# Kernel tuning notes

Measured on AMD Instinct MI355X. Metric: run time of the kernel, lower is better.

The kernel has to match this reference:

```python
import jax, jax.numpy as jnp
import numpy as np

DEPTH = 3

def _rx(theta):
    c, s = jnp.cos(theta / 2), jnp.sin(theta / 2)
    return jnp.stack([jnp.stack([c + 0j, -1j * s], -1),
                      jnp.stack([-1j * s, c + 0j], -1)], -2)

def _ry(theta):
    c, s = jnp.cos(theta / 2), jnp.sin(theta / 2)
    return jnp.stack([jnp.stack([c + 0j, -s + 0j], -1),
                      jnp.stack([s + 0j, c + 0j], -1)], -2)

def _rz(theta):
    e = jnp.exp(-0.5j * theta.astype(jnp.complex64))
    z = jnp.zeros_like(e)
    return jnp.stack([jnp.stack([e, z], -1),
                      jnp.stack([z, jnp.conj(e)], -1)], -2)

def _apply_1q(state, U, q):
    # state: (batch, 2,2,...,2); wire q lives on axis q+1. U: (2,2) or (batch,2,2)
    s = jnp.moveaxis(state, q + 1, -1)
    if U.ndim == 3:
        s = jnp.einsum('b...i,bji->b...j', s, U)
    else:
        s = jnp.einsum('...i,ji->...j', s, U)
    return jnp.moveaxis(s, -1, q + 1)

def _apply_cnot(state, c, t):
    s = jnp.moveaxis(state, (c + 1, t + 1), (-2, -1))
    s = jnp.concatenate([s[..., 0:1, :], s[..., 1:2, ::-1]], axis=-2)
    return jnp.moveaxis(s, (-2, -1), (c + 1, t + 1))

def _circuit(x, params):
    batch, n = x.shape
    depth = params.shape[0]
    state = jnp.zeros((batch,) + (2,) * n, jnp.complex64)
    state = state.at[(slice(None),) + (0,) * n].set(1.0)
    # data-encoding RX with per-sample angles
    for q in range(n):
        state = _apply_1q(state, _rx(x[:, q].astype(jnp.complex64).real), q)
    for l in range(depth):
        for q in range(n):
            state = _apply_1q(state, _rx(params[l, q, 0]), q)
            state = _apply_1q(state, _ry(params[l, q, 1]), q)
            state = _apply_1q(state, _rz(params[l, q, 2]), q)
        for q in range(n - 1):
            state = _apply_cnot(state, q, q + 1)
        state = _apply_cnot(state, n - 1, 0)
    probs = state.real ** 2 + state.imag ** 2  # (batch, 2,...,2)
    exps = []
    for w in range(n):
        p = jnp.moveaxis(probs, w + 1, 1).reshape(batch, 2, -1).sum(-1)
        exps.append(p[:, 0] - p[:, 1])  # <Z_w> = P(0) - P(1)
    return jnp.stack(exps, axis=1)


def setup_inputs() -> dict:
    key = jax.random.key(0)
    k1, k2 = jax.random.split(key)
    batch, n = 128, 14
    x = jax.random.normal(k1, (batch, n), dtype=jnp.float32)
    params = jax.random.normal(k2, (DEPTH, n, 3), dtype=jnp.float32)
    return {"x": x, "params": params}


def reference(x, params):
    return _circuit(x, params)
```

## Files before the change

kernel.cpp:

```cpp
#include <hip/hip_runtime.h>

namespace {

using v2f = __attribute__((ext_vector_type(2))) float;

constexpr int NQ      = 14;
constexpr int NSTATES = 1 << NQ;
constexpr int BLOCK   = 1024;
constexpr int NWAVES  = BLOCK / 64;

constexpr unsigned cparity(unsigned x){ x^=x>>8; x^=x>>4; x^=x>>2; x^=x>>1; return x&1u; }

struct Mat { unsigned row[NQ]; unsigned col[NQ]; };

constexpr Mat m_after(int nr){
  Mat m{};
  for(int p=0;p<NQ;++p){ m.row[p]=1u<<p; m.col[p]=1u<<p; }
  for(int l=0;l<nr;++l)
    for(int q=0;q<NQ;++q){
      int cq=(q==NQ-1)?NQ-1:q, tq=(q==NQ-1)?0:q+1;
      int Pc=NQ-1-cq, Pt=NQ-1-tq;
      m.row[Pt]^=m.row[Pc]; m.col[Pc]^=m.col[Pt];
    }
  return m;
}

constexpr Mat M1=m_after(1), M2=m_after(2), M3=m_after(3);
constexpr unsigned amask(int q){ return M1.col[NQ-1-q]; }
constexpr unsigned arow (int q){ return M1.row[NQ-1-q]; }
constexpr unsigned bmask(int q){ return M2.col[NQ-1-q]; }
constexpr unsigned brow (int q){ return M2.row[NQ-1-q]; }

constexpr int rank_of(const unsigned* v, int n){
  unsigned a[24]{};
  for(int i=0;i<n;++i) a[i]=v[i];
  int r=0;
  for(int bit=15;bit>=0;--bit){
    int p=-1;
    for(int i=r;i<n;++i){ if((a[i]>>bit)&1){ p=i; break; } }
    if(p<0) continue;
    unsigned t=a[r]; a[r]=a[p]; a[p]=t;
    for(int i=0;i<n;++i) if(i!=r && ((a[i]>>bit)&1)) a[i]^=a[r];
    ++r;
  }
  return r;
}

constexpr unsigned swzf(unsigned s, int k){ return s ^ ((s>>k)&31u); }

constexpr int proj_rank4(const unsigned* cols, int n, int k){
  unsigned a[8]{};
  for(int i=0;i<n;++i) a[i]=swzf(cols[i],k)&15u;
  int r=0;
  for(int bit=3;bit>=0;--bit){
    int p=-1;
    for(int i=r;i<n;++i){ if((a[i]>>bit)&1){ p=i; break; } }
    if(p<0) continue;
    unsigned t=a[r]; a[r]=a[p]; a[p]=t;
    for(int i=0;i<n;++i) if(i!=r && ((a[i]>>bit)&1)) a[i]^=a[r];
    ++r;
  }
  return r;
}

struct Plan {
  unsigned A[14], B[14], C[14];
  int BlaneGi[6]; unsigned BlanePi4[6];
  int BregGi[4];  unsigned BregEps[4];
  int CregGi[4];  unsigned CregEps[4];
  int ClaneGi[4]; unsigned ClaneEps[4];
  unsigned EJ4[14], ET[14];
  int K;
  unsigned SA[16], SB[16], SC[16];
  unsigned TA[10], TB[10], TCc[10];
};

constexpr Plan make_plan(){
  Plan P{};
  for(int t=0;t<14;++t) P.A[t]=amask(t);
  for(int t=0;t<4;++t){ P.B[t]=amask(10+t); P.BregGi[t]=10+t; }
  bool used[14]{}; int picked[14]{}; int np=0;
  {
    unsigned cur[20]{}; int nc=0;
    for(int t=0;t<4;++t) cur[nc++]=P.B[t];
    for(int q=0;q<14 && np<10;++q){
      cur[nc]=bmask(q);
      if(rank_of(cur,nc+1)==nc+1){ ++nc; picked[np++]=q; used[q]=true; }
    }
  }
  for(int i=0;i<6;++i){ P.B[4+i]=bmask(picked[i]); P.BlaneGi[i]=14+picked[i]; }
  int wq[4]{}, un[4]{}; int nu=0;
  for(int i=0;i<4;++i){ wq[i]=picked[6+i]; P.B[10+i]=bmask(wq[i]); P.CregGi[i]=14+wq[i]; }
  for(int q=0;q<14;++q) if(!used[q]) un[nu++]=q;
  for(int i=0;i<4;++i) P.ClaneGi[i]=14+un[i];
  for(int i=0;i<4;++i){ unsigned m=0;
    for(int t=0;t<10;++t) m |= cparity(arow(10+i)&P.B[4+t])<<t;
    P.BregEps[i]=m; }
  for(int i=0;i<6;++i){ unsigned m=0;
    for(int t=0;t<4;++t) m |= cparity(brow(picked[i])&P.B[t])<<t;
    P.BlanePi4[i]=m; }
  for(int t=0;t<4;++t) P.C[t]=bmask(wq[t]);
  for(int t=0;t<4;++t) P.C[4+t]=bmask(un[t]);
  {
    unsigned cc[20]{}; int n=0;
    for(int t=0;t<8;++t) cc[n++]=P.C[t];
    int pos=8;
    for(int p=0;p<14 && pos<14;++p){
      cc[n]=1u<<p;
      if(rank_of(cc,n+1)==n+1){ P.C[pos]=1u<<p; ++n; ++pos; }
    }
  }
  for(int i=0;i<4;++i){ unsigned m=0;
    for(int t=0;t<10;++t) m |= cparity(brow(wq[i])&P.C[4+t])<<t;
    P.CregEps[i]=m; }
  for(int i=0;i<4;++i){ unsigned m=0;
    for(int t=0;t<10;++t){ if(t==i) continue; m |= cparity(brow(un[i])&P.C[4+t])<<t; }
    P.ClaneEps[i]=m; }
  for(int w=0;w<14;++w){
    unsigned R=M3.row[NQ-1-w]; unsigned mj=0, mt=0;
    for(int t=0;t<4;++t)  mj |= cparity(R&P.C[t])<<t;
    for(int t=0;t<10;++t) mt |= cparity(R&P.C[4+t])<<t;
    P.EJ4[w]=mj; P.ET[w]=mt;
  }
  int bestk=2, bests=-1;
  for(int k=2;k<=9;++k){
    unsigned ini[6]={16,32,64,128,256,512};
    int s = proj_rank4(ini,6,k) + proj_rank4(&P.A[4],6,k)
          + proj_rank4(&P.B[4],6,k) + proj_rank4(&P.C[4],6,k);
    if(s>bests){ bests=s; bestk=k; }
  }
  P.K=bestk;
  for(int j=0;j<16;++j){
    unsigned sa=0, sb=0, sc=0;
    for(int t=0;t<4;++t) if((j>>t)&1){ sa^=P.A[t]; sb^=P.B[t]; sc^=P.C[t]; }
    P.SA[j]=swzf(sa,bestk); P.SB[j]=swzf(sb,bestk); P.SC[j]=swzf(sc,bestk);
  }
  for(int t=0;t<10;++t){
    P.TA[t]=swzf(P.A[4+t],bestk);
    P.TB[t]=swzf(P.B[4+t],bestk);
    P.TCc[t]=swzf(P.C[4+t],bestk);
  }
  return P;
}

constexpr Plan PL = make_plan();
static_assert(rank_of(PL.A,14)==14, "phase A map not bijective");
static_assert(rank_of(PL.B,14)==14, "phase B map not bijective");
static_assert(rank_of(PL.C,14)==14, "phase C map not bijective");

__device__ __forceinline__ v2f mkv(float a, float b){ v2f r; r[0]=a; r[1]=b; return r; }

__device__ __forceinline__ v2f pk_mul(v2f a, v2f b){
  v2f d; asm("v_pk_mul_f32 %0, %1, %2 op_sel:[0,0] op_sel_hi:[1,1]" : "=v"(d) : "v"(a), "v"(b)); return d;
}
__device__ __forceinline__ v2f pk_fma(v2f a, v2f b, v2f c){
  v2f d; asm("v_pk_fma_f32 %0, %1, %2, %3 op_sel:[0,0,0] op_sel_hi:[1,1,1]" : "=v"(d) : "v"(a), "v"(b), "v"(c)); return d;
}
__device__ __forceinline__ v2f pk_fma_swap1(v2f a, v2f b, v2f c){
  v2f d; asm("v_pk_fma_f32 %0, %1, %2, %3 op_sel:[0,1,0] op_sel_hi:[1,0,1]" : "=v"(d) : "v"(a), "v"(b), "v"(c)); return d;
}
__device__ __forceinline__ v2f cmul_pk(v2f uxx, v2f uyn, v2f s){ return pk_fma_swap1(uyn, s, pk_mul(uxx, s)); }
__device__ __forceinline__ v2f cfma_pk(v2f uxx, v2f uyn, v2f s, v2f acc){ return pk_fma_swap1(uyn, s, pk_fma(uxx, s, acc)); }

__device__ __forceinline__ float2 cmulf(float2 a, float2 b){
  return make_float2(a.x*b.x - a.y*b.y, a.x*b.y + a.y*b.x);
}
__device__ __forceinline__ v2f sel2(bool c, v2f x, v2f y){ v2f r; r[0]=c?x[0]:y[0]; r[1]=c?x[1]:y[1]; return r; }

struct GC { v2f u00x,u00n,u01x,u01n,u10x,u10n,u11x,u11n; };
__device__ __forceinline__ GC load_gc(const v2f* __restrict__ g){
  GC c{g[0],g[1],g[2],g[3],g[4],g[5],g[6],g[7]}; return c;
}

template<int KIND, int CTRL>
__device__ __forceinline__ v2f xchg(v2f v, int bpa){
  int x0=__float_as_int(v[0]), x1=__float_as_int(v[1]);
  int y0, y1;
  if constexpr (KIND==0){
    y0=__builtin_amdgcn_update_dpp(0,x0,CTRL,0xF,0xF,true);
    y1=__builtin_amdgcn_update_dpp(0,x1,CTRL,0xF,0xF,true);
  } else if constexpr (KIND==1){
    y0=__builtin_amdgcn_ds_swizzle(x0,CTRL);
    y1=__builtin_amdgcn_ds_swizzle(x1,CTRL);
  } else {
    y0=__builtin_amdgcn_ds_bpermute(bpa,x0);
    y1=__builtin_amdgcn_ds_bpermute(bpa,x1);
  }
  v2f r; r[0]=__int_as_float(y0); r[1]=__int_as_float(y1); return r;
}

template<int BIT>
__device__ __forceinline__ void reg_gate(v2f (&a)[16], const GC& c, bool eps){
  v2f m00x=sel2(eps,c.u11x,c.u00x), m00n=sel2(eps,c.u11n,c.u00n);
  v2f m01x=sel2(eps,c.u10x,c.u01x), m01n=sel2(eps,c.u10n,c.u01n);
  v2f m10x=sel2(eps,c.u01x,c.u10x), m10n=sel2(eps,c.u01n,c.u10n);
  v2f m11x=sel2(eps,c.u00x,c.u11x), m11n=sel2(eps,c.u00n,c.u11n);
#pragma unroll
  for(int v=0; v<16; ++v){
    if(!((v>>BIT)&1)){
      int w = v | (1<<BIT);
      v2f a0=a[v], a1=a[w];
      a[v] = cfma_pk(m01x,m01n,a1, cmul_pk(m00x,m00n,a0));
      a[w] = cfma_pk(m11x,m11n,a1, cmul_pk(m10x,m10n,a0));
    }
  }
}

template<int KIND, int CTRL, unsigned PI4>
__device__ __forceinline__ void lane_gate(v2f (&a)[16], const GC& c, bool sel, int bpa){
  v2f kax0=sel2(sel,c.u11x,c.u00x), kan0=sel2(sel,c.u11n,c.u00n);
  v2f kbx0=sel2(sel,c.u10x,c.u01x), kbn0=sel2(sel,c.u10n,c.u01n);
  v2f kax1=sel2(sel,c.u00x,c.u11x), kan1=sel2(sel,c.u00n,c.u11n);
  v2f kbx1=sel2(sel,c.u01x,c.u10x), kbn1=sel2(sel,c.u01n,c.u10n);
#pragma unroll
  for(int j=0;j<16;++j){
    v2f th = xchg<KIND,CTRL>(a[j], bpa);
    bool pi = (__builtin_popcount(PI4 & (unsigned)j) & 1) != 0;
    v2f kax = pi?kax1:kax0, kan = pi?kan1:kan0;
    v2f kbx = pi?kbx1:kbx0, kbn = pi?kbn1:kbn0;
    a[j] = cfma_pk(kbx,kbn,th, cmul_pk(kax,kan,a[j]));
  }
}

__device__ __forceinline__ unsigned base10(unsigned tid, const unsigned (&tc)[10]){
  unsigned s=0;
#pragma unroll
  for(int t=0;t<10;++t) s ^= tc[t] & (0u - ((tid>>t)&1u));
  return s;
}

__global__ void prep_gates(const float* __restrict__ prm, float* __restrict__ wsf){
  int t = threadIdx.x;
  if(t >= 2*NQ) return;
  int l = 1 + t/NQ, q = t % NQ;
  float ax=prm[(l*NQ+q)*3+0], ay=prm[(l*NQ+q)*3+1], az=prm[(l*NQ+q)*3+2];
  float cx,sx,cy,sy,cz,sz;
  sincosf(0.5f*ax,&sx,&cx); sincosf(0.5f*ay,&sy,&cy); sincosf(0.5f*az,&sz,&cz);
  float2 M00=make_float2(cy*cx, sy*sx),  M01=make_float2(-sy*cx,-cy*sx);
  float2 M10=make_float2(sy*cx,-cy*sx),  M11=make_float2(cy*cx,-sy*sx);
  float2 ez =make_float2(cz,-sz), ezc=make_float2(cz,sz);
  float2 U00=cmulf(ez,M00), U01=cmulf(ez,M01), U10=cmulf(ezc,M10), U11=cmulf(ezc,M11);
  float* o = wsf + t*16;
  o[0]=U00.x; o[1]=U00.x; o[2]=-U00.y; o[3]=U00.y;
  o[4]=U01.x; o[5]=U01.x; o[6]=-U01.y; o[7]=U01.y;
  o[8]=U10.x; o[9]=U10.x; o[10]=-U10.y; o[11]=U10.y;
  o[12]=U11.x; o[13]=U11.x; o[14]=-U11.y; o[15]=U11.y;
}

__global__ __launch_bounds__(BLOCK, 4) void qsim_kernel(
    const float* __restrict__ x,
    const float* __restrict__ prm,
    const v2f*  __restrict__ gw,
    float* __restrict__ out)
{
  __shared__ v2f    st[NSTATES];
  __shared__ float2 l0c[NQ][2];
  __shared__ float  red[NWAVES][NQ];

  const int b   = blockIdx.x;
  const unsigned tid = threadIdx.x;
  const int bpa = (int)((((tid&63u)^32u)<<2));

  if(tid < NQ){
    int q = tid;
    float ax = prm[q*3+0] + x[b*NQ+q];
    float ay = prm[q*3+1], az = prm[q*3+2];
    float cx,sx,cy,sy,cz,sz;
    sincosf(0.5f*ax,&sx,&cx); sincosf(0.5f*ay,&sy,&cy); sincosf(0.5f*az,&sz,&cz);
    l0c[q][0] = cmulf(make_float2(cz,-sz), make_float2(cy*cx,  sy*sx));
    l0c[q][1] = cmulf(make_float2(cz, sz), make_float2(sy*cx, -cy*sx));
  }
  __syncthreads();

  {
    float2 Pk = l0c[0][(tid>>9)&1];
#pragma unroll
    for(int q=1;q<10;++q) Pk = cmulf(Pk, l0c[q][(tid>>(9-q))&1]);
    float2 t2[2], t4[4];
    t2[0]=cmulf(Pk,l0c[10][0]); t2[1]=cmulf(Pk,l0c[10][1]);
#pragma unroll
    for(int i=0;i<2;++i){ t4[2*i]=cmulf(t2[i],l0c[11][0]); t4[2*i+1]=cmulf(t2[i],l0c[11][1]); }
#pragma unroll
    for(int j=0;j<16;++j){
      float2 v = cmulf(cmulf(t4[j>>2], l0c[12][(j>>1)&1]), l0c[13][j&1]);
      unsigned s = (tid<<4) | (unsigned)j;
      unsigned slot = s ^ ((s>>PL.K)&31u);
      st[slot] = mkv(v.x, v.y);
    }
  }
  __syncthreads();

  {
    unsigned sb = base10(tid, PL.TA);
    v2f a[16];
#pragma unroll
    for(int j=0;j<16;++j) a[j] = st[sb ^ PL.SA[j]];
    reg_gate<0>(a, load_gc(gw+0*8), false);
    reg_gate<1>(a, load_gc(gw+1*8), false);
    reg_gate<2>(a, load_gc(gw+2*8), false);
    reg_gate<3>(a, load_gc(gw+3*8), false);
    lane_gate<0,0xB1,  0u>(a, load_gc(gw+4*8), (tid&1)!=0,  bpa);
    lane_gate<0,0x4E,  0u>(a, load_gc(gw+5*8), (tid&2)!=0,  bpa);
    lane_gate<1,0x101F,0u>(a, load_gc(gw+6*8), (tid&4)!=0,  bpa);
    lane_gate<1,0x201F,0u>(a, load_gc(gw+7*8), (tid&8)!=0,  bpa);
    lane_gate<1,0x401F,0u>(a, load_gc(gw+8*8), (tid&16)!=0, bpa);
    lane_gate<2,0,     0u>(a, load_gc(gw+9*8), (tid&32)!=0, bpa);
#pragma unroll
    for(int j=0;j<16;++j) st[sb ^ PL.SA[j]] = a[j];
  }
  __syncthreads();

  {
    unsigned sb = base10(tid, PL.TB);
    v2f a[16];
#pragma unroll
    for(int j=0;j<16;++j) a[j] = st[sb ^ PL.SB[j]];
    reg_gate<0>(a, load_gc(gw+PL.BregGi[0]*8), (__builtin_popcount(PL.BregEps[0]&tid)&1)!=0);
    reg_gate<1>(a, load_gc(gw+PL.BregGi[1]*8), (__builtin_popcount(PL.BregEps[1]&tid)&1)!=0);
    reg_gate<2>(a, load_gc(gw+PL.BregGi[2]*8), (__builtin_popcount(PL.BregEps[2]&tid)&1)!=0);
    reg_gate<3>(a, load_gc(gw+PL.BregGi[3]*8), (__builtin_popcount(PL.BregEps[3]&tid)&1)!=0);
    lane_gate<0,0xB1,  PL.BlanePi4[0]>(a, load_gc(gw+PL.BlaneGi[0]*8), (tid&1)!=0,  bpa);
    lane_gate<0,0x4E,  PL.BlanePi4[1]>(a, load_gc(gw+PL.BlaneGi[1]*8), (tid&2)!=0,  bpa);
    lane_gate<1,0x101F,PL.BlanePi4[2]>(a, load_gc(gw+PL.BlaneGi[2]*8), (tid&4)!=0,  bpa);
    lane_gate<1,0x201F,PL.BlanePi4[3]>(a, load_gc(gw+PL.BlaneGi[3]*8), (tid&8)!=0,  bpa);
    lane_gate<1,0x401F,PL.BlanePi4[4]>(a, load_gc(gw+PL.BlaneGi[4]*8), (tid&16)!=0, bpa);
    lane_gate<2,0,     PL.BlanePi4[5]>(a, load_gc(gw+PL.BlaneGi[5]*8), (tid&32)!=0, bpa);
#pragma unroll
    for(int j=0;j<16;++j) st[sb ^ PL.SB[j]] = a[j];
  }
  __syncthreads();

  {
    unsigned sb = base10(tid, PL.TCc);
    v2f a[16];
#pragma unroll
    for(int j=0;j<16;++j) a[j] = st[sb ^ PL.SC[j]];
    reg_gate<0>(a, load_gc(gw+PL.CregGi[0]*8), (__builtin_popcount(PL.CregEps[0]&tid)&1)!=0);
    reg_gate<1>(a, load_gc(gw+PL.CregGi[1]*8), (__builtin_popcount(PL.CregEps[1]&tid)&1)!=0);
    reg_gate<2>(a, load_gc(gw+PL.CregGi[2]*8), (__builtin_popcount(PL.CregEps[2]&tid)&1)!=0);
    reg_gate<3>(a, load_gc(gw+PL.CregGi[3]*8), (__builtin_popcount(PL.CregEps[3]&tid)&1)!=0);
    lane_gate<0,0xB1,  0u>(a, load_gc(gw+PL.ClaneGi[0]*8),
        (((tid&1u)!=0) != ((__builtin_popcount(PL.ClaneEps[0]&tid)&1)!=0)), bpa);
    lane_gate<0,0x4E,  0u>(a, load_gc(gw+PL.ClaneGi[1]*8),
        (((tid&2u)!=0) != ((__builtin_popcount(PL.ClaneEps[1]&tid)&1)!=0)), bpa);
    lane_gate<1,0x101F,0u>(a, load_gc(gw+PL.ClaneGi[2]*8),
        (((tid&4u)!=0) != ((__builtin_popcount(PL.ClaneEps[2]&tid)&1)!=0)), bpa);
    lane_gate<1,0x201F,0u>(a, load_gc(gw+PL.ClaneGi[3]*8),
        (((tid&8u)!=0) != ((__builtin_popcount(PL.ClaneEps[3]&tid)&1)!=0)), bpa);

    float acc[NQ];
#pragma unroll
    for(int w=0;w<NQ;++w) acc[w]=0.f;
#pragma unroll
    for(int j=0;j<16;++j){
      float p = a[j][0]*a[j][0] + a[j][1]*a[j][1];
#pragma unroll
      for(int w=0;w<NQ;++w){
        if(__builtin_popcount(PL.EJ4[w] & (unsigned)j) & 1) acc[w]-=p; else acc[w]+=p;
      }
    }
    const int lane = tid & 63, wave = tid >> 6;
#pragma unroll
    for(int w=0;w<NQ;++w){
      float v = (__builtin_popcount(PL.ET[w]&tid)&1) ? -acc[w] : acc[w];
#pragma unroll
      for(int off=32; off>0; off>>=1) v += __shfl_down(v, off, 64);
      if(lane==0) red[wave][w]=v;
    }
    __syncthreads();
    if(tid < NQ){
      float s=0.f;
#pragma unroll
      for(int wv=0; wv<NWAVES; ++wv) s += red[wv][tid];
      out[b*NQ + tid] = s;
    }
  }
}

}

extern "C" void kernel_launch(void* const* d_in, const int* in_sizes, int n_in,
                              void* d_out, int out_size, void* d_ws, size_t ws_size,
                              hipStream_t stream) {
  const float* x   = (const float*)d_in[0];
  const float* prm = (const float*)d_in[1];
  float* out = (float*)d_out;
  const int batch = in_sizes[0] / NQ;
  prep_gates<<<1, 64, 0, stream>>>(prm, (float*)d_ws);
  qsim_kernel<<<batch, BLOCK, 0, stream>>>(x, prm, (const v2f*)d_ws, out);
}
```

Baseline: 42.59 us.

## Replace XOR-swizzled shared state with padded scatter layout and cache gate tables in LDS

Removes the XOR-swizzle addressing of the shared state vector. Each phase now reads its 16 amplitudes contiguously from a row padded to stride 17, then scatters results into the next phase's layout through compile-time inverse basis maps. This needs an extra barrier before each scatter. Gate matrices are staged into shared memory instead of being read from global memory. Lane exchanges switch from ds_bpermute and one ds_swizzle to DPP row_shr-style moves and permlane32_swap, cutting LDS-based shuffles at the cost of a larger shared footprint (17K v2f).

```diff
diff --git a/kernel.cpp b/kernel.cpp
--- a/kernel.cpp
+++ b/kernel.cpp
@@ -46,23 +46,6 @@
   return r;
 }
 
-constexpr unsigned swzf(unsigned s, int k){ return s ^ ((s>>k)&31u); }
-
-constexpr int proj_rank4(const unsigned* cols, int n, int k){
-  unsigned a[8]{};
-  for(int i=0;i<n;++i) a[i]=swzf(cols[i],k)&15u;
-  int r=0;
-  for(int bit=3;bit>=0;--bit){
-    int p=-1;
-    for(int i=r;i<n;++i){ if((a[i]>>bit)&1){ p=i; break; } }
-    if(p<0) continue;
-    unsigned t=a[r]; a[r]=a[p]; a[p]=t;
-    for(int i=0;i<n;++i) if(i!=r && ((a[i]>>bit)&1)) a[i]^=a[r];
-    ++r;
-  }
-  return r;
-}
-
 struct Plan {
   unsigned A[14], B[14], C[14];
   int BlaneGi[6]; unsigned BlanePi4[6];
@@ -70,9 +53,6 @@
   int CregGi[4];  unsigned CregEps[4];
   int ClaneGi[4]; unsigned ClaneEps[4];
   unsigned EJ4[14], ET[14];
-  int K;
-  unsigned SA[16], SB[16], SC[16];
-  unsigned TA[10], TB[10], TCc[10];
 };
 
 constexpr Plan make_plan(){
@@ -122,24 +102,6 @@
     for(int t=0;t<10;++t) mt |= cparity(R&P.C[4+t])<<t;
     P.EJ4[w]=mj; P.ET[w]=mt;
   }
-  int bestk=2, bests=-1;
-  for(int k=2;k<=9;++k){
-    unsigned ini[6]={16,32,64,128,256,512};
-    int s = proj_rank4(ini,6,k) + proj_rank4(&P.A[4],6,k)
-          + proj_rank4(&P.B[4],6,k) + proj_rank4(&P.C[4],6,k);
-    if(s>bests){ bests=s; bestk=k; }
-  }
-  P.K=bestk;
-  for(int j=0;j<16;++j){
-    unsigned sa=0, sb=0, sc=0;
-    for(int t=0;t<4;++t) if((j>>t)&1){ sa^=P.A[t]; sb^=P.B[t]; sc^=P.C[t]; }
-    P.SA[j]=swzf(sa,bestk); P.SB[j]=swzf(sb,bestk); P.SC[j]=swzf(sc,bestk);
-  }
-  for(int t=0;t<10;++t){
-    P.TA[t]=swzf(P.A[4+t],bestk);
-    P.TB[t]=swzf(P.B[4+t],bestk);
-    P.TCc[t]=swzf(P.C[4+t],bestk);
-  }
   return P;
 }
 
@@ -148,6 +110,64 @@
 static_assert(rank_of(PL.B,14)==14, "phase B map not bijective");
 static_assert(rank_of(PL.C,14)==14, "phase C map not bijective");
 
+struct Inv { unsigned col[NQ]; };
+constexpr Inv inv_basis(const unsigned* bas){
+  unsigned vec[NQ]{}, cmb[NQ]{}; bool used[NQ]{}; int pivk[NQ]{};
+  for(int k=0;k<NQ;++k){ vec[k]=bas[k]; cmb[k]=1u<<k; }
+  for(int b=0;b<NQ;++b){
+    int p=-1;
+    for(int k=0;k<NQ;++k) if(!used[k] && ((vec[k]>>b)&1)){ p=k; break; }
+    used[p]=true; pivk[b]=p;
+    for(int k=0;k<NQ;++k) if(k!=p && ((vec[k]>>b)&1)){ vec[k]^=vec[p]; cmb[k]^=cmb[p]; }
+  }
+  Inv R{};
+  for(int b=0;b<NQ;++b) R.col[b]=cmb[pivk[b]];
+  return R;
+}
+constexpr bool check_inv(const unsigned* bas, const Inv& iv){
+  for(int p=0;p<NQ;++p){
+    unsigned s=0;
+    for(int k=0;k<NQ;++k) if((iv.col[p]>>k)&1) s^=bas[k];
+    if(s != (1u<<p)) return false;
+  }
+  return true;
+}
+constexpr Inv IA = inv_basis(PL.A), IB = inv_basis(PL.B), IC = inv_basis(PL.C);
+static_assert(check_inv(PL.A, IA), "IA");
+static_assert(check_inv(PL.B, IB), "IB");
+static_assert(check_inv(PL.C, IC), "IC");
+
+struct Trans { unsigned t[NQ]; };
+constexpr Trans trans_phys(const Inv& iv){
+  Trans T{};
+  for(int p=0;p<NQ;++p) T.t[p]=iv.col[p];
+  return T;
+}
+constexpr Trans trans_of(const unsigned* cur, const Inv& iv){
+  Trans T{};
+  for(int k=0;k<NQ;++k){
+    unsigned c=0;
+    for(int p=0;p<NQ;++p) if((cur[k]>>p)&1) c^=iv.col[p];
+    T.t[k]=c;
+  }
+  return T;
+}
+constexpr Trans T_PA = trans_phys(IA);
+constexpr Trans T_AB = trans_of(PL.A, IB);
+constexpr Trans T_BC = trans_of(PL.B, IC);
+
+struct CJ { unsigned v[16]; };
+constexpr CJ mk_cj(const Trans& T){
+  CJ c{};
+  for(int j=0;j<16;++j){
+    unsigned s=0;
+    for(int b=0;b<4;++b) if((j>>b)&1) s^=T.t[b];
+    c.v[j]=s;
+  }
+  return c;
+}
+constexpr CJ CJ_PA=mk_cj(T_PA), CJ_AB=mk_cj(T_AB), CJ_BC=mk_cj(T_BC);
+
 __device__ __forceinline__ v2f mkv(float a, float b){ v2f r; r[0]=a; r[1]=b; return r; }
 
 __device__ __forceinline__ v2f pk_mul(v2f a, v2f b){
@@ -172,20 +192,30 @@
   GC c{g[0],g[1],g[2],g[3],g[4],g[5],g[6],g[7]}; return c;
 }
 
-template<int KIND, int CTRL>
-__device__ __forceinline__ v2f xchg(v2f v, int bpa){
+template<int CTRL>
+__device__ __forceinline__ int dpp(int x){
+  return __builtin_amdgcn_update_dpp(0, x, CTRL, 0xF, 0xF, true);
+}
+__device__ __forceinline__ int x32(int x, unsigned lane){
+  auto r = __builtin_amdgcn_permlane32_swap((unsigned)x, (unsigned)x, false, false);
+  return (lane & 32u) ? (int)r[0] : (int)r[1];
+}
+template<int K>
+__device__ __forceinline__ v2f xpart(v2f v, unsigned lane){
   int x0=__float_as_int(v[0]), x1=__float_as_int(v[1]);
   int y0, y1;
-  if constexpr (KIND==0){
-    y0=__builtin_amdgcn_update_dpp(0,x0,CTRL,0xF,0xF,true);
-    y1=__builtin_amdgcn_update_dpp(0,x1,CTRL,0xF,0xF,true);
-  } else if constexpr (KIND==1){
-    y0=__builtin_amdgcn_ds_swizzle(x0,CTRL);
-    y1=__builtin_amdgcn_ds_swizzle(x1,CTRL);
-  } else {
-    y0=__builtin_amdgcn_ds_bpermute(bpa,x0);
-    y1=__builtin_amdgcn_ds_bpermute(bpa,x1);
-  }
+  if constexpr (K==0){ y0=dpp<0xB1>(x0);  y1=dpp<0xB1>(x1); }
+  else if constexpr (K==1){ y0=dpp<0x4E>(x0);  y1=dpp<0x4E>(x1); }
+  else if constexpr (K==2){
+    y0=__builtin_amdgcn_ds_swizzle(x0,0x101F);
+    y1=__builtin_amdgcn_ds_swizzle(x1,0x101F);
+  }
+  else if constexpr (K==3){ y0=dpp<0x128>(x0); y1=dpp<0x128>(x1); }
+  else if constexpr (K==4){
+    y0=__builtin_amdgcn_ds_swizzle(x0,0x401F);
+    y1=__builtin_amdgcn_ds_swizzle(x1,0x401F);
+  }
+  else { y0=x32(x0,lane); y1=x32(x1,lane); }
   v2f r; r[0]=__int_as_float(y0); r[1]=__int_as_float(y1); return r;
 }
 
@@ -206,15 +236,15 @@
   }
 }
 
-template<int KIND, int CTRL, unsigned PI4>
-__device__ __forceinline__ void lane_gate(v2f (&a)[16], const GC& c, bool sel, int bpa){
+template<int XK, unsigned PI4>
+__device__ __forceinline__ void lane_gate(v2f (&a)[16], const GC& c, bool sel, unsigned lane){
   v2f kax0=sel2(sel,c.u11x,c.u00x), kan0=sel2(sel,c.u11n,c.u00n);
   v2f kbx0=sel2(sel,c.u10x,c.u01x), kbn0=sel2(sel,c.u10n,c.u01n);
   v2f kax1=sel2(sel,c.u00x,c.u11x), kan1=sel2(sel,c.u00n,c.u11n);
   v2f kbx1=sel2(sel,c.u01x,c.u10x), kbn1=sel2(sel,c.u01n,c.u10n);
 #pragma unroll
   for(int j=0;j<16;++j){
-    v2f th = xchg<KIND,CTRL>(a[j], bpa);
+    v2f th = xpart<XK>(a[j], lane);
     bool pi = (__builtin_popcount(PI4 & (unsigned)j) & 1) != 0;
     v2f kax = pi?kax1:kax0, kan = pi?kan1:kan0;
     v2f kbx = pi?kbx1:kbx0, kbn = pi?kbn1:kbn0;
@@ -222,11 +252,20 @@
   }
 }
 
-__device__ __forceinline__ unsigned base10(unsigned tid, const unsigned (&tc)[10]){
+__device__ __forceinline__ unsigned nb_of(unsigned tid, const unsigned (&t)[NQ]){
   unsigned s=0;
 #pragma unroll
-  for(int t=0;t<10;++t) s ^= tc[t] & (0u - ((tid>>t)&1u));
+  for(int k=0;k<10;++k) s ^= t[4+k] & (0u-((tid>>k)&1u));
   return s;
+}
+
+__device__ __forceinline__ void scatter16(v2f* __restrict__ st, const v2f (&a)[16],
+                                          unsigned nb, const CJ& cj){
+#pragma unroll
+  for(int j=0;j<16;++j){
+    unsigned d = nb ^ cj.v[j];
+    st[d + (d>>4)] = a[j];
+  }
 }
 
 __global__ void prep_gates(const float* __restrict__ prm, float* __restrict__ wsf){
@@ -250,17 +289,19 @@
 __global__ __launch_bounds__(BLOCK, 4) void qsim_kernel(
     const float* __restrict__ x,
     const float* __restrict__ prm,
-    const v2f*  __restrict__ gw,
+    const float* __restrict__ gw,
     float* __restrict__ out)
 {
-  __shared__ v2f    st[NSTATES];
+  __shared__ v2f    st[BLOCK*17];
+  __shared__ v2f    Utab[28*8];
   __shared__ float2 l0c[NQ][2];
   __shared__ float  red[NWAVES][NQ];
 
-  const int b   = blockIdx.x;
+  const int b = blockIdx.x;
   const unsigned tid = threadIdx.x;
-  const int bpa = (int)((((tid&63u)^32u)<<2));
-
+  const unsigned lane = tid & 63u;
+
+  if(tid < 28*16) ((float*)Utab)[tid] = gw[tid];
   if(tid < NQ){
     int q = tid;
     float ax = prm[q*3+0] + x[b*NQ+q];
@@ -280,73 +321,73 @@
     t2[0]=cmulf(Pk,l0c[10][0]); t2[1]=cmulf(Pk,l0c[10][1]);
 #pragma unroll
     for(int i=0;i<2;++i){ t4[2*i]=cmulf(t2[i],l0c[11][0]); t4[2*i+1]=cmulf(t2[i],l0c[11][1]); }
+    v2f a[16];
 #pragma unroll
     for(int j=0;j<16;++j){
       float2 v = cmulf(cmulf(t4[j>>2], l0c[12][(j>>1)&1]), l0c[13][j&1]);
-      unsigned s = (tid<<4) | (unsigned)j;
-      unsigned slot = s ^ ((s>>PL.K)&31u);
-      st[slot] = mkv(v.x, v.y);
-    }
+      a[j] = mkv(v.x, v.y);
+    }
+    scatter16(st, a, nb_of(tid, T_PA.t), CJ_PA);
   }
   __syncthreads();
 
   {
-    unsigned sb = base10(tid, PL.TA);
     v2f a[16];
-#pragma unroll
-    for(int j=0;j<16;++j) a[j] = st[sb ^ PL.SA[j]];
-    reg_gate<0>(a, load_gc(gw+0*8), false);
-    reg_gate<1>(a, load_gc(gw+1*8), false);
-    reg_gate<2>(a, load_gc(gw+2*8), false);
-    reg_gate<3>(a, load_gc(gw+3*8), false);
-    lane_gate<0,0xB1,  0u>(a, load_gc(gw+4*8), (tid&1)!=0,  bpa);
-    lane_gate<0,0x4E,  0u>(a, load_gc(gw+5*8), (tid&2)!=0,  bpa);
-    lane_gate<1,0x101F,0u>(a, load_gc(gw+6*8), (tid&4)!=0,  bpa);
-    lane_gate<1,0x201F,0u>(a, load_gc(gw+7*8), (tid&8)!=0,  bpa);
-    lane_gate<1,0x401F,0u>(a, load_gc(gw+8*8), (tid&16)!=0, bpa);
-    lane_gate<2,0,     0u>(a, load_gc(gw+9*8), (tid&32)!=0, bpa);
-#pragma unroll
-    for(int j=0;j<16;++j) st[sb ^ PL.SA[j]] = a[j];
+    const int rb = (int)tid*17;
+#pragma unroll
+    for(int j=0;j<16;++j) a[j] = st[rb + j];
+    reg_gate<0>(a, load_gc(Utab+0*8), false);
+    reg_gate<1>(a, load_gc(Utab+1*8), false);
+    reg_gate<2>(a, load_gc(Utab+2*8), false);
+    reg_gate<3>(a, load_gc(Utab+3*8), false);
+    lane_gate<0,0u>(a, load_gc(Utab+4*8), (tid&1)!=0,  lane);
+    lane_gate<1,0u>(a, load_gc(Utab+5*8), (tid&2)!=0,  lane);
+    lane_gate<2,0u>(a, load_gc(Utab+6*8), (tid&4)!=0,  lane);
+    lane_gate<3,0u>(a, load_gc(Utab+7*8), (tid&8)!=0,  lane);
+    lane_gate<4,0u>(a, load_gc(Utab+8*8), (tid&16)!=0, lane);
+    lane_gate<5,0u>(a, load_gc(Utab+9*8), (tid&32)!=0, lane);
+    __syncthreads();
+    scatter16(st, a, nb_of(tid, T_AB.t), CJ_AB);
   }
   __syncthreads();
 
   {
-    unsigned sb = base10(tid, PL.TB);
     v2f a[16];
-#pragma unroll
-    for(int j=0;j<16;++j) a[j] = st[sb ^ PL.SB[j]];
-    reg_gate<0>(a, load_gc(gw+PL.BregGi[0]*8), (__builtin_popcount(PL.BregEps[0]&tid)&1)!=0);
-    reg_gate<1>(a, load_gc(gw+PL.BregGi[1]*8), (__builtin_popcount(PL.BregEps[1]&tid)&1)!=0);
-    reg_gate<2>(a, load_gc(gw+PL.BregGi[2]*8), (__builtin_popcount(PL.BregEps[2]&tid)&1)!=0);
-    reg_gate<3>(a, load_gc(gw+PL.BregGi[3]*8), (__builtin_popcount(PL.BregEps[3]&tid)&1)!=0);
-    lane_gate<0,0xB1,  PL.BlanePi4[0]>(a, load_gc(gw+PL.BlaneGi[0]*8), (tid&1)!=0,  bpa);
-    lane_gate<0,0x4E,  PL.BlanePi4[1]>(a, load_gc(gw+PL.BlaneGi[1]*8), (tid&2)!=0,  bpa);
-    lane_gate<1,0x101F,PL.BlanePi4[2]>(a, load_gc(gw+PL.BlaneGi[2]*8), (tid&4)!=0,  bpa);
-    lane_gate<1,0x201F,PL.BlanePi4[3]>(a, load_gc(gw+PL.BlaneGi[3]*8), (tid&8)!=0,  bpa);
-    lane_gate<1,0x401F,PL.BlanePi4[4]>(a, load_gc(gw+PL.BlaneGi[4]*8), (tid&16)!=0, bpa);
-    lane_gate<2,0,     PL.BlanePi4[5]>(a, load_gc(gw+PL.BlaneGi[5]*8), (tid&32)!=0, bpa);
-#pragma unroll
-    for(int j=0;j<16;++j) st[sb ^ PL.SB[j]] = a[j];
+    const int rb = (int)tid*17;
+#pragma unroll
+    for(int j=0;j<16;++j) a[j] = st[rb + j];
+    reg_gate<0>(a, load_gc(Utab+PL.BregGi[0]*8), (__builtin_popcount(PL.BregEps[0]&tid)&1)!=0);
+    reg_gate<1>(a, load_gc(Utab+PL.BregGi[1]*8), (__builtin_popcount(PL.BregEps[1]&tid)&1)!=0);
+    reg_gate<2>(a, load_gc(Utab+PL.BregGi[2]*8), (__builtin_popcount(PL.BregEps[2]&tid)&1)!=0);
+    reg_gate<3>(a, load_gc(Utab+PL.BregGi[3]*8), (__builtin_popcount(PL.BregEps[3]&tid)&1)!=0);
+    lane_gate<0,PL.BlanePi4[0]>(a, load_gc(Utab+PL.BlaneGi[0]*8), (tid&1)!=0,  lane);
+    lane_gate<1,PL.BlanePi4[1]>(a, load_gc(Utab+PL.BlaneGi[1]*8), (tid&2)!=0,  lane);
+    lane_gate<2,PL.BlanePi4[2]>(a, load_gc(Utab+PL.BlaneGi[2]*8), (tid&4)!=0,  lane);
+    lane_gate<3,PL.BlanePi4[3]>(a, load_gc(Utab+PL.BlaneGi[3]*8), (tid&8)!=0,  lane);
+    lane_gate<4,PL.BlanePi4[4]>(a, load_gc(Utab+PL.BlaneGi[4]*8), (tid&16)!=0, lane);
+    lane_gate<5,PL.BlanePi4[5]>(a, load_gc(Utab+PL.BlaneGi[5]*8), (tid&32)!=0, lane);
+    __syncthreads();
+    scatter16(st, a, nb_of(tid, T_BC.t), CJ_BC);
   }
   __syncthreads();
 
   {
-    unsigned sb = base10(tid, PL.TCc);
     v2f a[16];
-#pragma unroll
-    for(int j=0;j<16;++j) a[j] = st[sb ^ PL.SC[j]];
-    reg_gate<0>(a, load_gc(gw+PL.CregGi[0]*8), (__builtin_popcount(PL.CregEps[0]&tid)&1)!=0);
-    reg_gate<1>(a, load_gc(gw+PL.CregGi[1]*8), (__builtin_popcount(PL.CregEps[1]&tid)&1)!=0);
-    reg_gate<2>(a, load_gc(gw+PL.CregGi[2]*8), (__builtin_popcount(PL.CregEps[2]&tid)&1)!=0);
-    reg_gate<3>(a, load_gc(gw+PL.CregGi[3]*8), (__builtin_popcount(PL.CregEps[3]&tid)&1)!=0);
-    lane_gate<0,0xB1,  0u>(a, load_gc(gw+PL.ClaneGi[0]*8),
-        (((tid&1u)!=0) != ((__builtin_popcount(PL.ClaneEps[0]&tid)&1)!=0)), bpa);
-    lane_gate<0,0x4E,  0u>(a, load_gc(gw+PL.ClaneGi[1]*8),
-        (((tid&2u)!=0) != ((__builtin_popcount(PL.ClaneEps[1]&tid)&1)!=0)), bpa);
-    lane_gate<1,0x101F,0u>(a, load_gc(gw+PL.ClaneGi[2]*8),
-        (((tid&4u)!=0) != ((__builtin_popcount(PL.ClaneEps[2]&tid)&1)!=0)), bpa);
-    lane_gate<1,0x201F,0u>(a, load_gc(gw+PL.ClaneGi[3]*8),
-        (((tid&8u)!=0) != ((__builtin_popcount(PL.ClaneEps[3]&tid)&1)!=0)), bpa);
+    const int rb = (int)tid*17;
+#pragma unroll
+    for(int j=0;j<16;++j) a[j] = st[rb + j];
+    reg_gate<0>(a, load_gc(Utab+PL.CregGi[0]*8), (__builtin_popcount(PL.CregEps[0]&tid)&1)!=0);
+    reg_gate<1>(a, load_gc(Utab+PL.CregGi[1]*8), (__builtin_popcount(PL.CregEps[1]&tid)&1)!=0);
+    reg_gate<2>(a, load_gc(Utab+PL.CregGi[2]*8), (__builtin_popcount(PL.CregEps[2]&tid)&1)!=0);
+    reg_gate<3>(a, load_gc(Utab+PL.CregGi[3]*8), (__builtin_popcount(PL.CregEps[3]&tid)&1)!=0);
+    lane_gate<0,0u>(a, load_gc(Utab+PL.ClaneGi[0]*8),
+        (((tid&1u)!=0) != ((__builtin_popcount(PL.ClaneEps[0]&tid)&1)!=0)), lane);
+    lane_gate<1,0u>(a, load_gc(Utab+PL.ClaneGi[1]*8),
+        (((tid&2u)!=0) != ((__builtin_popcount(PL.ClaneEps[1]&tid)&1)!=0)), lane);
+    lane_gate<2,0u>(a, load_gc(Utab+PL.ClaneGi[2]*8),
+        (((tid&4u)!=0) != ((__builtin_popcount(PL.ClaneEps[2]&tid)&1)!=0)), lane);
+    lane_gate<3,0u>(a, load_gc(Utab+PL.ClaneGi[3]*8),
+        (((tid&8u)!=0) != ((__builtin_popcount(PL.ClaneEps[3]&tid)&1)!=0)), lane);
 
     float acc[NQ];
 #pragma unroll
@@ -359,7 +400,7 @@
         if(__builtin_popcount(PL.EJ4[w] & (unsigned)j) & 1) acc[w]-=p; else acc[w]+=p;
       }
     }
-    const int lane = tid & 63, wave = tid >> 6;
+    const int wave = tid >> 6;
 #pragma unroll
     for(int w=0;w<NQ;++w){
       float v = (__builtin_popcount(PL.ET[w]&tid)&1) ? -acc[w] : acc[w];
@@ -387,5 +428,5 @@
   float* out = (float*)d_out;
   const int batch = in_sizes[0] / NQ;
   prep_gates<<<1, 64, 0, stream>>>(prm, (float*)d_ws);
-  qsim_kernel<<<batch, BLOCK, 0, stream>>>(x, prm, (const v2f*)d_ws, out);
-}
+  qsim_kernel<<<batch, BLOCK, 0, stream>>>(x, prm, (const float*)d_ws, out);
+}
```

After: 43.67 us. +2.5%, slower.
